# Optimization experiments

Measured on AMD Instinct MI355X. Metric: run time of the kernel, lower is better.

The kernel has to match this reference:

```python
import jax, jax.numpy as jnp
import numpy as np

N_THRESH = 100  # thresholds = 0.00, 0.01, ..., 0.99


def setup_inputs() -> dict:
    key = jax.random.key(0)
    k1, k2 = jax.random.split(key)
    predicted_mask = jax.random.uniform(k1, (32, 1, 1024, 1024), dtype=jnp.float32)
    gt_mask = jax.random.randint(k2, (32, 1, 1024, 1024), 0, 2, dtype=jnp.int32)
    return {"predicted_mask": predicted_mask, "gt_mask": gt_mask}


def reference(predicted_mask, gt_mask):
    # Single-pass histogram formulation of: for each t_k in arange(0,1,0.01),
    # iou_k = |(pred > t_k) & gt| / |(pred > t_k) | gt|  (torchmetrics binary Jaccard,
    # strict '>' thresholding, safe-divide -> 0 when union is empty).
    thresholds = jnp.arange(0.0, 1.0, 0.01, dtype=jnp.float32)  # [100], sorted
    pred = jnp.squeeze(predicted_mask).ravel()                  # [N] probabilities in [0,1]
    gt = jnp.squeeze(gt_mask).ravel().astype(jnp.float32)       # [N] 0/1

    # cnt[i] = number of thresholds strictly below pred[i]; pixel i satisfies
    # (pred > t_k) exactly for k in [0, cnt[i]).
    cnt = jnp.searchsorted(thresholds, pred, side='left')       # [N] int in [0, 100]

    hist_pos = jax.ops.segment_sum(gt, cnt, num_segments=N_THRESH + 1)              # [101]
    hist_all = jax.ops.segment_sum(jnp.ones_like(gt), cnt, num_segments=N_THRESH + 1)

    # TP_k = #{pred > t_k and gt==1} = sum_{c > k} hist_pos[c]  (suffix sums via cumsum)
    tp = jnp.sum(hist_pos) - jnp.cumsum(hist_pos)[:N_THRESH]        # [100]
    pred_pos = jnp.sum(hist_all) - jnp.cumsum(hist_all)[:N_THRESH]  # [100] #{pred > t_k}
    n_gt_pos = jnp.sum(gt)

    union = pred_pos + n_gt_pos - tp                                 # TP + FP + FN
    ious = jnp.where(union > 0, tp / jnp.maximum(union, 1.0), 0.0)   # safe divide -> 0
    return thresholds, ious
```

## Files before the change

### kernel.cpp

```cpp
#include <hip/hip_runtime.h>

#define N_THRESH 100
#define NBINS 101

__global__ void zero_ws_kernel(unsigned long long* __restrict__ ws) {
    int i = threadIdx.x;
    if (i < NBINS) ws[i] = 0ull;
}

__global__ __launch_bounds__(256) void hist_kernel(
        const float* __restrict__ pred,
        const int* __restrict__ gt,
        unsigned long long* __restrict__ ws,
        int n) {
    __shared__ unsigned long long hist[4][NBINS];
    __shared__ float thr[NBINS + 1];

    const int tid  = threadIdx.x;
    const int wave = tid >> 6;

    for (int i = tid; i < 4 * NBINS; i += blockDim.x)
        (&hist[0][0])[i] = 0ull;
    if (tid <= N_THRESH)
        thr[tid] = (tid == N_THRESH) ? 2.0f : (float)((double)tid * 0.01);
    __syncthreads();

    const int nvec = n >> 2;
    const float4* __restrict__ p4 = (const float4*)pred;
    const int4*   __restrict__ g4 = (const int4*)gt;
    const int stride = gridDim.x * blockDim.x;

    for (int i = blockIdx.x * blockDim.x + tid; i < nvec; i += stride) {
        float4 p = p4[i];
        int4   g = g4[i];
        float pv[4] = {p.x, p.y, p.z, p.w};
        int   gv[4] = {g.x, g.y, g.z, g.w};
#pragma unroll
        for (int j = 0; j < 4; ++j) {
            float v = pv[j];
            int c = (int)(v * 100.0f) + 1;
            c = c < 0 ? 0 : (c > N_THRESH ? N_THRESH : c);
            while (c > 0 && thr[c - 1] >= v) --c;
            while (thr[c] < v) ++c;
            unsigned long long add =
                ((unsigned long long)(gv[j] != 0) << 32) | 1ull;
            atomicAdd(&hist[wave][c], add);
        }
    }

    if (blockIdx.x == 0 && tid == 0) {
        for (int i = nvec << 2; i < n; ++i) {
            float v = pred[i];
            int c = (int)(v * 100.0f) + 1;
            c = c < 0 ? 0 : (c > N_THRESH ? N_THRESH : c);
            while (c > 0 && thr[c - 1] >= v) --c;
            while (thr[c] < v) ++c;
            unsigned long long add =
                ((unsigned long long)(gt[i] != 0) << 32) | 1ull;
            atomicAdd(&hist[0][c], add);
        }
    }

    __syncthreads();
    if (tid < NBINS) {
        unsigned long long s = hist[0][tid] + hist[1][tid]
                             + hist[2][tid] + hist[3][tid];
        if (s) atomicAdd(&ws[tid], s);
    }
}

__global__ void finalize_kernel(const unsigned long long* __restrict__ ws,
                                float* __restrict__ out) {
    __shared__ unsigned int pos[NBINS], all[NBINS];
    int k = threadIdx.x;
    if (k < NBINS) {
        unsigned long long h = ws[k];
        pos[k] = (unsigned int)(h >> 32);
        all[k] = (unsigned int)(h & 0xffffffffull);
    }
    __syncthreads();
    if (k < N_THRESH) {
        out[k] = (float)((double)k * 0.01);
        unsigned long long tp = 0, pp = 0, ngt = 0;
        for (int c = k + 1; c <= N_THRESH; ++c) { tp += pos[c]; pp += all[c]; }
        for (int c = 0; c <= N_THRESH; ++c) ngt += pos[c];
        long long uni = (long long)(pp + ngt - tp);
        double iou = (uni > 0) ? (double)tp / (double)uni : 0.0;
        out[N_THRESH + k] = (float)iou;
    }
}

extern "C" void kernel_launch(void* const* d_in, const int* in_sizes, int n_in,
                              void* d_out, int out_size, void* d_ws, size_t ws_size,
                              hipStream_t stream) {
    const float* pred = (const float*)d_in[0];
    const int*   gt   = (const int*)d_in[1];
    float* out = (float*)d_out;
    unsigned long long* ws = (unsigned long long*)d_ws;
    int n = in_sizes[0];

    zero_ws_kernel<<<1, 128, 0, stream>>>(ws);
    hist_kernel<<<2048, 256, 0, stream>>>(pred, gt, ws, n);
    finalize_kernel<<<1, 128, 0, stream>>>(ws, out);
}
```

Before: 302.9 us.

## Compute threshold bins arithmetically, split shared histograms per lane parity, unroll loads

Replaces the shared-memory threshold table and its while-loop search with a closed-form bin computation that compares against two recomputed double-derived thresholds. Doubles the shared sub-histograms from one per wave to one per wave and lane parity, which is meant to cut LDS atomic contention. Also processes two grid-stride elements per iteration to put more loads in flight. The costs are double-precision arithmetic per element and a larger shared footprint.

```diff
diff --git a/kernel.cpp b/kernel.cpp
--- a/kernel.cpp
+++ b/kernel.cpp
@@ -2,10 +2,30 @@
 
 #define N_THRESH 100
 #define NBINS 101
+#define NSUB 8
 
 __global__ void zero_ws_kernel(unsigned long long* __restrict__ ws) {
     int i = threadIdx.x;
     if (i < NBINS) ws[i] = 0ull;
+}
+
+__device__ __forceinline__ int bin_of(float v) {
+    int e = (int)(v * 100.0f);
+    e = e < 0 ? 0 : (e > 99 ? 99 : e);
+    double ed = (double)e * 0.01;
+    float t0 = (float)ed;
+    float t1 = (float)(ed + 0.01);
+    int c = e + (t0 < v ? 1 : 0) + (t1 < v ? 1 : 0);
+    return c > N_THRESH ? N_THRESH : c;
+}
+
+__device__ __forceinline__ void accum4(unsigned long long* __restrict__ h,
+                                       float4 p, int4 g) {
+    int c0 = bin_of(p.x), c1 = bin_of(p.y), c2 = bin_of(p.z), c3 = bin_of(p.w);
+    atomicAdd(&h[c0], ((unsigned long long)(g.x != 0) << 32) | 1ull);
+    atomicAdd(&h[c1], ((unsigned long long)(g.y != 0) << 32) | 1ull);
+    atomicAdd(&h[c2], ((unsigned long long)(g.z != 0) << 32) | 1ull);
+    atomicAdd(&h[c3], ((unsigned long long)(g.w != 0) << 32) | 1ull);
 }
 
 __global__ __launch_bounds__(256) void hist_kernel(
@@ -13,58 +33,47 @@
         const int* __restrict__ gt,
         unsigned long long* __restrict__ ws,
         int n) {
-    __shared__ unsigned long long hist[4][NBINS];
-    __shared__ float thr[NBINS + 1];
+    __shared__ unsigned long long hist[NSUB][NBINS];
 
-    const int tid  = threadIdx.x;
-    const int wave = tid >> 6;
+    const int tid = threadIdx.x;
+    const int sub = ((tid >> 6) << 1) | (tid & 1);
+    unsigned long long* __restrict__ h = hist[sub];
 
-    for (int i = tid; i < 4 * NBINS; i += blockDim.x)
+    for (int i = tid; i < NSUB * NBINS; i += blockDim.x)
         (&hist[0][0])[i] = 0ull;
-    if (tid <= N_THRESH)
-        thr[tid] = (tid == N_THRESH) ? 2.0f : (float)((double)tid * 0.01);
     __syncthreads();
 
     const int nvec = n >> 2;
     const float4* __restrict__ p4 = (const float4*)pred;
     const int4*   __restrict__ g4 = (const int4*)gt;
-    const int stride = gridDim.x * blockDim.x;
+    const int gsz = gridDim.x * blockDim.x;
 
-    for (int i = blockIdx.x * blockDim.x + tid; i < nvec; i += stride) {
-        float4 p = p4[i];
-        int4   g = g4[i];
-        float pv[4] = {p.x, p.y, p.z, p.w};
-        int   gv[4] = {g.x, g.y, g.z, g.w};
-#pragma unroll
-        for (int j = 0; j < 4; ++j) {
-            float v = pv[j];
-            int c = (int)(v * 100.0f) + 1;
-            c = c < 0 ? 0 : (c > N_THRESH ? N_THRESH : c);
-            while (c > 0 && thr[c - 1] >= v) --c;
-            while (thr[c] < v) ++c;
-            unsigned long long add =
-                ((unsigned long long)(gv[j] != 0) << 32) | 1ull;
-            atomicAdd(&hist[wave][c], add);
-        }
+    int i = blockIdx.x * blockDim.x + tid;
+    for (; i + gsz < nvec; i += 2 * gsz) {
+        float4 pa = p4[i];
+        int4   ga = g4[i];
+        float4 pb = p4[i + gsz];
+        int4   gb = g4[i + gsz];
+        accum4(h, pa, ga);
+        accum4(h, pb, gb);
+    }
+    for (; i < nvec; i += gsz) {
+        accum4(h, p4[i], g4[i]);
     }
 
     if (blockIdx.x == 0 && tid == 0) {
-        for (int i = nvec << 2; i < n; ++i) {
-            float v = pred[i];
-            int c = (int)(v * 100.0f) + 1;
-            c = c < 0 ? 0 : (c > N_THRESH ? N_THRESH : c);
-            while (c > 0 && thr[c - 1] >= v) --c;
-            while (thr[c] < v) ++c;
-            unsigned long long add =
-                ((unsigned long long)(gt[i] != 0) << 32) | 1ull;
-            atomicAdd(&hist[0][c], add);
+        for (int k = nvec << 2; k < n; ++k) {
+            int c = bin_of(pred[k]);
+            atomicAdd(&hist[0][c],
+                      ((unsigned long long)(gt[k] != 0) << 32) | 1ull);
         }
     }
 
     __syncthreads();
     if (tid < NBINS) {
-        unsigned long long s = hist[0][tid] + hist[1][tid]
-                             + hist[2][tid] + hist[3][tid];
+        unsigned long long s = 0ull;
+#pragma unroll
+        for (int w = 0; w < NSUB; ++w) s += hist[w][tid];
         if (s) atomicAdd(&ws[tid], s);
     }
 }
```

Measured after the change: 284.8 us. -6.0%, faster.
